# Performance work log

Measured on AMD Instinct MI355X. Metric: run time of the kernel, lower is better.

## Reference

```python
import jax, jax.numpy as jnp
import numpy as np

SIGMA = 0.25  # self.sigmas in RBFDynamics


def setup_inputs() -> dict:
    key = jax.random.key(0)
    k1, k2, k3 = jax.random.split(key, 3)
    N, C, D, M = 100000, 256, 2, 5
    x = jax.random.normal(k1, (N, D), dtype=jnp.float32)
    centers = jax.random.normal(k2, (C, D), dtype=jnp.float32)
    weights = jax.random.normal(k3, (M, C, D), dtype=jnp.float32)
    return {"x": x, "centers": centers, "weights": weights}


def reference(x, centers, weights):
    x2 = jnp.sum(x * x, axis=-1, keepdims=True)          # [N, 1]
    c2 = jnp.sum(centers * centers, axis=-1)             # [C]
    d2 = x2 + c2[None, :] - 2.0 * (x @ centers.T)        # [N, C]
    d2 = jnp.maximum(d2, 0.0)
    # torch: exp(-cdist(x, centers)**2) * sigmas**2
    rbf = jnp.exp(-d2) * (SIGMA * SIGMA)                 # [N, C]
    # per-model matmul with weights, batched across ensemble -> [M, N, D]
    out = jnp.einsum('nc,mcd->mnd', rbf, weights)
    return out
```

## Files before the change

kernel.cpp:

```cpp
#include <hip/hip_runtime.h>

#if __has_builtin(__builtin_amdgcn_exp2f)
__device__ __forceinline__ float fast_exp2(float x) { return __builtin_amdgcn_exp2f(x); }
#else
__device__ __forceinline__ float fast_exp2(float x) { return exp2f(x); }
#endif

constexpr int C_ = 256;
constexpr int M_ = 5;
constexpr float LOG2E = 1.4426950408889634f;

__global__ __launch_bounds__(256) void ensemble_rbf_kernel(
    const float* __restrict__ x,
    const float* __restrict__ centers,
    const float* __restrict__ weights,
    float* __restrict__ out,
    int N)
{
    __shared__ float s_tab[C_ * 12];

    const int tid   = threadIdx.x;
    const int nl    = tid & 63;
    const int chunk = tid >> 6;

    {
        float2 cv = ((const float2*)centers)[tid];
        float* row = &s_tab[tid * 12];
        row[0] = cv.x;
        row[1] = cv.y;
        const float2* w2 = (const float2*)weights;
        #pragma unroll
        for (int m = 0; m < M_; m++) {
            float2 wv = w2[m * C_ + tid];
            row[2 + 2 * m]     = wv.x;
            row[2 + 2 * m + 1] = wv.y;
        }
    }
    __syncthreads();

    const int n = blockIdx.x * 64 + nl;
    float2 xv = (n < N) ? ((const float2*)x)[n] : make_float2(0.f, 0.f);

    float accx[M_], accy[M_];
    #pragma unroll
    for (int m = 0; m < M_; m++) { accx[m] = 0.f; accy[m] = 0.f; }

    const float4* tab4 = (const float4*)s_tab;
    const int cbase = chunk * 64;

    #pragma unroll 8
    for (int cc = 0; cc < 64; cc++) {
        int c = cbase + cc;
        float4 t0 = tab4[c * 3 + 0];
        float4 t1 = tab4[c * 3 + 1];
        float4 t2 = tab4[c * 3 + 2];

        float dx = xv.x - t0.x;
        float dy = xv.y - t0.y;
        float d2 = fmaf(dx, dx, dy * dy);
        float r  = fast_exp2(fmaf(d2, -LOG2E, -4.0f));

        accx[0] = fmaf(r, t0.z, accx[0]);  accy[0] = fmaf(r, t0.w, accy[0]);
        accx[1] = fmaf(r, t1.x, accx[1]);  accy[1] = fmaf(r, t1.y, accy[1]);
        accx[2] = fmaf(r, t1.z, accx[2]);  accy[2] = fmaf(r, t1.w, accy[2]);
        accx[3] = fmaf(r, t2.x, accx[3]);  accy[3] = fmaf(r, t2.y, accy[3]);
        accx[4] = fmaf(r, t2.z, accx[4]);  accy[4] = fmaf(r, t2.w, accy[4]);
    }

    __syncthreads();
    {
        float4* slot = (float4*)&s_tab[(chunk * 64 + nl) * 12];
        slot[0] = make_float4(accx[0], accy[0], accx[1], accy[1]);
        slot[1] = make_float4(accx[2], accy[2], accx[3], accy[3]);
        slot[2] = make_float4(accx[4], accy[4], 0.f, 0.f);
    }
    __syncthreads();

    if (tid < 64 && n < N) {
        float4 s0 = make_float4(0.f, 0.f, 0.f, 0.f);
        float4 s1 = s0, s2 = s0;
        #pragma unroll
        for (int k = 0; k < 4; k++) {
            const float4* slot = (const float4*)&s_tab[(k * 64 + nl) * 12];
            float4 r0 = slot[0], r1 = slot[1], r2 = slot[2];
            s0.x += r0.x; s0.y += r0.y; s0.z += r0.z; s0.w += r0.w;
            s1.x += r1.x; s1.y += r1.y; s1.z += r1.z; s1.w += r1.w;
            s2.x += r2.x; s2.y += r2.y;
        }
        float2* out2 = (float2*)out;
        out2[(size_t)0 * N + n] = make_float2(s0.x, s0.y);
        out2[(size_t)1 * N + n] = make_float2(s0.z, s0.w);
        out2[(size_t)2 * N + n] = make_float2(s1.x, s1.y);
        out2[(size_t)3 * N + n] = make_float2(s1.z, s1.w);
        out2[(size_t)4 * N + n] = make_float2(s2.x, s2.y);
    }
}

extern "C" void kernel_launch(void* const* d_in, const int* in_sizes, int n_in,
                              void* d_out, int out_size, void* d_ws, size_t ws_size,
                              hipStream_t stream) {
    const float* x       = (const float*)d_in[0];
    const float* centers = (const float*)d_in[1];
    const float* weights = (const float*)d_in[2];
    float* out = (float*)d_out;

    int N = in_sizes[0] / 2;
    int grid = (N + 63) / 64;
    ensemble_rbf_kernel<<<grid, 256, 0, stream>>>(x, centers, weights, out, N);
}
```

Before: 69.97 us.

## Factor RBF exponent into per-point and per-center terms, inner loop uses dot product

Expands exp(-|x-c|^2) into exp(-|x|^2) * exp(-|c|^2) * exp(2 x·c). The per-center factor and the sigma^2 scale are folded into the shared-memory weight table, and the per-point factor is applied once at output, so the inner loop computes only a two-term dot product before exp2. It also sets launch_bounds occupancy to 8 and lowers unroll from 8 to 4. The factored form can lose precision or overflow or underflow when |x| or |c| is large, because the separate exponentials may leave float range even where the true product is finite.

```diff
diff --git a/kernel.cpp b/kernel.cpp
--- a/kernel.cpp
+++ b/kernel.cpp
@@ -10,7 +10,7 @@
 constexpr int M_ = 5;
 constexpr float LOG2E = 1.4426950408889634f;
 
-__global__ __launch_bounds__(256) void ensemble_rbf_kernel(
+__global__ __launch_bounds__(256, 8) void ensemble_rbf_kernel(
     const float* __restrict__ x,
     const float* __restrict__ centers,
     const float* __restrict__ weights,
@@ -25,15 +25,17 @@
 
     {
         float2 cv = ((const float2*)centers)[tid];
+        float c2  = fmaf(cv.x, cv.x, cv.y * cv.y);
+        float s   = fast_exp2(fmaf(c2, -LOG2E, -4.0f));
         float* row = &s_tab[tid * 12];
-        row[0] = cv.x;
-        row[1] = cv.y;
+        row[0] = (2.0f * LOG2E) * cv.x;
+        row[1] = (2.0f * LOG2E) * cv.y;
         const float2* w2 = (const float2*)weights;
         #pragma unroll
         for (int m = 0; m < M_; m++) {
             float2 wv = w2[m * C_ + tid];
-            row[2 + 2 * m]     = wv.x;
-            row[2 + 2 * m + 1] = wv.y;
+            row[2 + 2 * m]     = wv.x * s;
+            row[2 + 2 * m + 1] = wv.y * s;
         }
     }
     __syncthreads();
@@ -41,38 +43,35 @@
     const int n = blockIdx.x * 64 + nl;
     float2 xv = (n < N) ? ((const float2*)x)[n] : make_float2(0.f, 0.f);
 
-    float accx[M_], accy[M_];
+    float acc[2 * M_];
     #pragma unroll
-    for (int m = 0; m < M_; m++) { accx[m] = 0.f; accy[m] = 0.f; }
+    for (int i = 0; i < 2 * M_; i++) acc[i] = 0.f;
 
     const float4* tab4 = (const float4*)s_tab;
     const int cbase = chunk * 64;
 
-    #pragma unroll 8
+    #pragma unroll 4
     for (int cc = 0; cc < 64; cc++) {
         int c = cbase + cc;
         float4 t0 = tab4[c * 3 + 0];
         float4 t1 = tab4[c * 3 + 1];
         float4 t2 = tab4[c * 3 + 2];
 
-        float dx = xv.x - t0.x;
-        float dy = xv.y - t0.y;
-        float d2 = fmaf(dx, dx, dy * dy);
-        float r  = fast_exp2(fmaf(d2, -LOG2E, -4.0f));
+        float r = fast_exp2(fmaf(xv.y, t0.y, xv.x * t0.x));
 
-        accx[0] = fmaf(r, t0.z, accx[0]);  accy[0] = fmaf(r, t0.w, accy[0]);
-        accx[1] = fmaf(r, t1.x, accx[1]);  accy[1] = fmaf(r, t1.y, accy[1]);
-        accx[2] = fmaf(r, t1.z, accx[2]);  accy[2] = fmaf(r, t1.w, accy[2]);
-        accx[3] = fmaf(r, t2.x, accx[3]);  accy[3] = fmaf(r, t2.y, accy[3]);
-        accx[4] = fmaf(r, t2.z, accx[4]);  accy[4] = fmaf(r, t2.w, accy[4]);
+        acc[0] = fmaf(r, t0.z, acc[0]);  acc[1] = fmaf(r, t0.w, acc[1]);
+        acc[2] = fmaf(r, t1.x, acc[2]);  acc[3] = fmaf(r, t1.y, acc[3]);
+        acc[4] = fmaf(r, t1.z, acc[4]);  acc[5] = fmaf(r, t1.w, acc[5]);
+        acc[6] = fmaf(r, t2.x, acc[6]);  acc[7] = fmaf(r, t2.y, acc[7]);
+        acc[8] = fmaf(r, t2.z, acc[8]);  acc[9] = fmaf(r, t2.w, acc[9]);
     }
 
     __syncthreads();
     {
         float4* slot = (float4*)&s_tab[(chunk * 64 + nl) * 12];
-        slot[0] = make_float4(accx[0], accy[0], accx[1], accy[1]);
-        slot[1] = make_float4(accx[2], accy[2], accx[3], accy[3]);
-        slot[2] = make_float4(accx[4], accy[4], 0.f, 0.f);
+        slot[0] = make_float4(acc[0], acc[1], acc[2], acc[3]);
+        slot[1] = make_float4(acc[4], acc[5], acc[6], acc[7]);
+        slot[2] = make_float4(acc[8], acc[9], 0.f, 0.f);
     }
     __syncthreads();
 
@@ -87,12 +86,15 @@
             s1.x += r1.x; s1.y += r1.y; s1.z += r1.z; s1.w += r1.w;
             s2.x += r2.x; s2.y += r2.y;
         }
+        float x2    = fmaf(xv.x, xv.x, xv.y * xv.y);
+        float scale = fast_exp2(x2 * -LOG2E);
+
         float2* out2 = (float2*)out;
-        out2[(size_t)0 * N + n] = make_float2(s0.x, s0.y);
-        out2[(size_t)1 * N + n] = make_float2(s0.z, s0.w);
-        out2[(size_t)2 * N + n] = make_float2(s1.x, s1.y);
-        out2[(size_t)3 * N + n] = make_float2(s1.z, s1.w);
-        out2[(size_t)4 * N + n] = make_float2(s2.x, s2.y);
+        out2[(size_t)0 * N + n] = make_float2(s0.x * scale, s0.y * scale);
+        out2[(size_t)1 * N + n] = make_float2(s0.z * scale, s0.w * scale);
+        out2[(size_t)2 * N + n] = make_float2(s1.x * scale, s1.y * scale);
+        out2[(size_t)3 * N + n] = make_float2(s1.z * scale, s1.w * scale);
+        out2[(size_t)4 * N + n] = make_float2(s2.x * scale, s2.y * scale);
     }
 }
 
```

Measured after the change: 70.19 us. Within noise of the previous version (+0.3%).
